# Kernel tuning notes

Hardware: AMD Instinct MI355X
Metric: run time of the kernel (lower is better)

Reference implementation:

```python
import jax, jax.numpy as jnp
import numpy as np

AUX_LOSS_WEIGHT = 0.01
TOP_K = 2


def setup_inputs() -> dict:
    key = jax.random.key(0)
    k0, k1, k2, k3, k4 = jax.random.split(key, 5)
    B, S, H, I, E = 4, 2048, 1024, 2816, 8
    scale = 0.02
    x = jax.random.normal(k0, (B, S, H), dtype=jnp.float32)
    Wr = jax.random.normal(k1, (H, E), dtype=jnp.float32) * scale   # router
    Wg = jax.random.normal(k2, (E, H, I), dtype=jnp.float32) * scale  # gate proj per expert
    Wu = jax.random.normal(k3, (E, H, I), dtype=jnp.float32) * scale  # up proj per expert
    Wd = jax.random.normal(k4, (E, I, H), dtype=jnp.float32) * scale  # down proj per expert
    return {"x": x, "Wr": Wr, "Wg": Wg, "Wu": Wu, "Wd": Wd}


def reference(x, Wr, Wg, Wu, Wd):
    B, S, H = x.shape
    E = Wr.shape[1]
    xf = x.reshape(-1, H)                      # [T, H]

    # Router: softmax -> top-k -> renormalize top-k weights
    logits = xf @ Wr                           # [T, E]
    probs = jax.nn.softmax(logits, axis=-1)
    vals, idx = jax.lax.top_k(probs, TOP_K)    # [T, K]
    vals = vals / (vals.sum(axis=-1, keepdims=True) + 1e-9)

    # Aux load-balancing loss (matches torch: mean prob * mean one-hot load)
    oh = jax.nn.one_hot(idx, E, dtype=xf.dtype)        # [T, K, E]
    expert_load = oh.sum(axis=1).mean(axis=0)          # [E]
    expert_prob = probs.mean(axis=0)                   # [E]
    router_loss = E * jnp.sum(expert_prob * expert_load) * AUX_LOSS_WEIGHT

    # Per-token combine weight for each expert: c[t,e] = sum_k vals[t,k] * (idx[t,k]==e)
    comb = jnp.einsum('tk,tke->te', vals, oh)          # [T, E]

    # Loop over the small fixed set of experts (dense SwiGLU, masked-weighted combine;
    # identical math to gather -> expert -> weighted index_add scatter)
    def expert_step(acc, ew):
        wg, wu, wd, ce = ew                            # [H,I], [H,I], [I,H], [T]
        h = jax.nn.silu(xf @ wg) * (xf @ wu)           # [T, I]
        return acc + (h @ wd) * ce[:, None], None

    out, _ = jax.lax.scan(expert_step, jnp.zeros_like(xf), (Wg, Wu, Wd, comb.T))
    return out.reshape(B, S, H), router_loss
```

## Files before the change

### kernel.cpp

```cpp
#include <hip/hip_runtime.h>
#include <stdint.h>

#define T_TOK 8192
#define HD    1024
#define ID    2816
#define NE    8
#define RCAP  17408

typedef __bf16 bf16x8 __attribute__((ext_vector_type(8)));
typedef float  f32x4  __attribute__((ext_vector_type(4)));

__device__ __forceinline__ unsigned short f2bf(float f) {
  union { float f; unsigned u; } v; v.f = f;
  unsigned r = v.u + 0x7FFFu + ((v.u >> 16) & 1u);
  return (unsigned short)(r >> 16);
}

__device__ __forceinline__ void gl16(const void* g, void* l) {
  __builtin_amdgcn_global_load_lds((__attribute__((address_space(1))) void*)g,
                                   (__attribute__((address_space(3))) void*)l,
                                   16, 0, 0);
}

__global__ void k_cvt_x(const float* __restrict__ x, unsigned short* __restrict__ xb) {
  const int i = blockIdx.x * blockDim.x + threadIdx.x;
  const float4 v = ((const float4*)x)[i];
  ushort4 o;
  o.x = f2bf(v.x); o.y = f2bf(v.y); o.z = f2bf(v.z); o.w = f2bf(v.w);
  ((ushort4*)xb)[i] = o;
}

__global__ void k_transpose(const float* __restrict__ Wg, const float* __restrict__ Wu,
                            const float* __restrict__ Wd,
                            unsigned short* __restrict__ Wgt, unsigned short* __restrict__ Wut,
                            unsigned short* __restrict__ Wdt) {
  const int m = blockIdx.y;
  const float* src; unsigned short* dst; int R, C;
  if (m < 8)       { src = Wg + (size_t)m * HD * ID;        dst = Wgt + (size_t)m * HD * ID;        R = HD; C = ID; }
  else if (m < 16) { src = Wu + (size_t)(m - 8) * HD * ID;  dst = Wut + (size_t)(m - 8) * HD * ID;  R = HD; C = ID; }
  else             { src = Wd + (size_t)(m - 16) * HD * ID; dst = Wdt + (size_t)(m - 16) * HD * ID; R = ID; C = HD; }
  const int tc = C / 64;
  const int tr = blockIdx.x / tc, tcc = blockIdx.x % tc;
  const int r0 = tr * 64, c0 = tcc * 64;
  __shared__ __align__(16) unsigned short tl[64 * 64];
  const int t = threadIdx.x;
  const int rb = t >> 4;
  const int c4 = t & 15;
  const float* sp = src + (size_t)(r0 + rb * 4) * C + c0 + c4 * 4;
  float4 v[4];
#pragma unroll
  for (int i = 0; i < 4; ++i) v[i] = *(const float4*)(sp + (size_t)i * C);
  const float* vf = (const float*)v;
#pragma unroll
  for (int q = 0; q < 4; ++q) {
    const int c = c4 * 4 + q;
    ushort4 o;
    o.x = f2bf(vf[0 * 4 + q]); o.y = f2bf(vf[1 * 4 + q]);
    o.z = f2bf(vf[2 * 4 + q]); o.w = f2bf(vf[3 * 4 + q]);
    *(ushort4*)&tl[c * 64 + ((rb ^ (c & 15)) * 4)] = o;
  }
  __syncthreads();
  const int orow = t >> 2, seg = t & 3;
  __align__(16) unsigned short tmp[16];
#pragma unroll
  for (int mI = 0; mI < 4; ++mI) {
    const int s = seg * 4 + mI;
    *(ushort4*)&tmp[mI * 4] = *(const ushort4*)&tl[orow * 64 + ((s ^ (orow & 15)) * 4)];
  }
  unsigned short* dp = dst + (size_t)(c0 + orow) * R + r0 + seg * 16;
  ((uint4*)dp)[0] = ((const uint4*)tmp)[0];
  ((uint4*)dp)[1] = ((const uint4*)tmp)[1];
}

__global__ void k_router(const float* __restrict__ x, const float* __restrict__ Wr,
                         int* __restrict__ cnt, float* __restrict__ psum,
                         int* __restrict__ tok_e, float* __restrict__ tok_w) {
  __shared__ float bp[NE];
  __shared__ int bc[NE];
  const int tid = threadIdx.x;
  if (tid < NE) { bp[tid] = 0.f; bc[tid] = 0; }
  __syncthreads();
  const int lane = tid & 63, w = tid >> 6;
  const int t = blockIdx.x * 4 + w;
  float acc[NE] = {0.f, 0.f, 0.f, 0.f, 0.f, 0.f, 0.f, 0.f};
  for (int h = lane; h < HD; h += 64) {
    const float xv = x[(size_t)t * HD + h];
    const float4 w0 = *(const float4*)(Wr + h * 8);
    const float4 w1 = *(const float4*)(Wr + h * 8 + 4);
    acc[0] += xv * w0.x; acc[1] += xv * w0.y; acc[2] += xv * w0.z; acc[3] += xv * w0.w;
    acc[4] += xv * w1.x; acc[5] += xv * w1.y; acc[6] += xv * w1.z; acc[7] += xv * w1.w;
  }
#pragma unroll
  for (int e = 0; e < NE; ++e)
    for (int off = 32; off > 0; off >>= 1)
      acc[e] += __shfl_xor(acc[e], off, 64);
  if (lane == 0) {
    float mx = acc[0];
    for (int e = 1; e < NE; ++e) mx = fmaxf(mx, acc[e]);
    float p[NE], s = 0.f;
    for (int e = 0; e < NE; ++e) { p[e] = __expf(acc[e] - mx); s += p[e]; }
    const float inv = 1.f / s;
    for (int e = 0; e < NE; ++e) p[e] *= inv;
    int e0 = 0;
    for (int e = 1; e < NE; ++e) if (p[e] > p[e0]) e0 = e;
    int e1 = (e0 == 0) ? 1 : 0;
    for (int e = 0; e < NE; ++e) if (e != e0 && p[e] > p[e1]) e1 = e;
    const float v0 = p[e0], v1 = p[e1];
    const float invs = 1.f / (v0 + v1 + 1e-9f);
    tok_e[2 * t] = e0;          tok_e[2 * t + 1] = e1;
    tok_w[2 * t] = v0 * invs;   tok_w[2 * t + 1] = v1 * invs;
    atomicAdd(&bc[e0], 1); atomicAdd(&bc[e1], 1);
    for (int e = 0; e < NE; ++e) atomicAdd(&bp[e], p[e]);
  }
  __syncthreads();
  if (tid < NE) { atomicAdd(&cnt[tid], bc[tid]); atomicAdd(&psum[tid], bp[tid]); }
}

__global__ void k_offsets(const int* __restrict__ cnt, const float* __restrict__ psum,
                          int* __restrict__ offp, int* __restrict__ pair_tok,
                          float* __restrict__ pair_w, float* __restrict__ loss_out) {
  __shared__ int soff[NE + 1], scnt[NE];
  if (threadIdx.x == 0) {
    int o = 0;
    for (int e = 0; e < NE; ++e) {
      soff[e] = o; scnt[e] = cnt[e];
      o += (scnt[e] + 127) & ~127;
    }
    soff[NE] = o;
    for (int e = 0; e <= NE; ++e) offp[e] = soff[e];
    float loss = 0.f;
    for (int e = 0; e < NE; ++e) loss += psum[e] * (float)scnt[e];
    loss *= (float)NE * 0.01f / ((float)T_TOK * (float)T_TOK);
    *loss_out = loss;
  }
  __syncthreads();
  for (int e = 0; e < NE; ++e) {
    const int base = soff[e] + scnt[e];
    const int n = soff[e + 1] - base;
    for (int j = threadIdx.x; j < n; j += blockDim.x) {
      pair_tok[base + j] = -1;
      pair_w[base + j] = 0.f;
    }
  }
}

__global__ void k_scatter(const int* __restrict__ tok_e, const float* __restrict__ tok_w,
                          const int* __restrict__ offp, int* __restrict__ cursor,
                          int* __restrict__ pair_tok, float* __restrict__ pair_w,
                          int* __restrict__ inv_p) {
  const int t = blockIdx.x * 256 + threadIdx.x;
#pragma unroll
  for (int k = 0; k < 2; ++k) {
    const int e = tok_e[2 * t + k];
    const int pos = atomicAdd(&cursor[e], 1);
    const int idx = offp[e] + pos;
    pair_tok[idx] = t;
    pair_w[idx] = tok_w[2 * t + k];
    inv_p[2 * t + k] = idx;
  }
}

__launch_bounds__(256, 2)
__global__ void k_stage1(const unsigned short* __restrict__ xb,
                         const unsigned short* __restrict__ Wgt,
                         const unsigned short* __restrict__ Wut,
                         const int* __restrict__ offp,
                         const int* __restrict__ pair_tok,
                         unsigned short* __restrict__ act) {
  __shared__ __align__(16) unsigned short lA[8192];
  __shared__ __align__(16) unsigned short lBg[8192];
  __shared__ __align__(16) unsigned short lBu[8192];
  __shared__ int toks[128];

  const int row0 = blockIdx.y * 128;
  if (row0 >= offp[8]) return;
  int e = 0;
  while (offp[e + 1] <= row0) ++e;
  const int i0 = blockIdx.x * 128;
  const int tid = threadIdx.x;
  if (tid < 128) {
    const int tk = pair_tok[row0 + tid];
    toks[tid] = tk < 0 ? 0 : tk;
  }
  __syncthreads();

  const int lane = tid & 63, w = tid >> 6;
  const unsigned short* gA[4];
  const unsigned short* gBg[4];
  const unsigned short* gBu[4];
  unsigned ldso[4];
  const unsigned short* wgtE = Wgt + (size_t)e * ID * HD;
  const unsigned short* wutE = Wut + (size_t)e * ID * HD;
#pragma unroll
  for (int j = 0; j < 4; ++j) {
    const int row = (w * 4 + j) * 8 + (lane >> 3);
    const int kb = (lane & 7) ^ (row & 7);
    gA[j]  = xb + (size_t)toks[row] * HD + kb * 8;
    gBg[j] = wgtE + (size_t)(i0 + row) * HD + kb * 8;
    gBu[j] = wutE + (size_t)(i0 + row) * HD + kb * 8;
    ldso[j] = (unsigned)(w * 4 + j) * 512u;
  }

  const f32x4 zero = {0.f, 0.f, 0.f, 0.f};
  f32x4 accg[4][4], accu[4][4];
#pragma unroll
  for (int a = 0; a < 4; ++a)
#pragma unroll
    for (int b = 0; b < 4; ++b) { accg[a][b] = zero; accu[a][b] = zero; }

  const int wm = (w & 1) * 64, wn = (w >> 1) * 64;
  const int colm = lane & 15, quad = lane >> 4;

  for (int kt = 0; kt < HD / 64; ++kt) {
    __syncthreads();
    const int ko = kt * 64;
#pragma unroll
    for (int j = 0; j < 4; ++j) {
      gl16(gA[j] + ko,  &lA[ldso[j]]);
      gl16(gBg[j] + ko, &lBg[ldso[j]]);
      gl16(gBu[j] + ko, &lBu[ldso[j]]);
    }
    __syncthreads();
#pragma unroll
    for (int kk = 0; kk < 2; ++kk) {
      const int kbl = kk * 4 + quad;
      bf16x8 af[4], bg[4], bu[4];
#pragma unroll
      for (int mf = 0; mf < 4; ++mf) {
        const int r = wm + mf * 16 + colm;
        af[mf] = *(const bf16x8*)&lA[r * 64 + ((kbl ^ (r & 7)) * 8)];
      }
#pragma unroll
      for (int nf = 0; nf < 4; ++nf) {
        const int r = wn + nf * 16 + colm;
        const int o = r * 64 + ((kbl ^ (r & 7)) * 8);
        bg[nf] = *(const bf16x8*)&lBg[o];
        bu[nf] = *(const bf16x8*)&lBu[o];
      }
#pragma unroll
      for (int mf = 0; mf < 4; ++mf)
#pragma unroll
        for (int nf = 0; nf < 4; ++nf) {
          accg[mf][nf] = __builtin_amdgcn_mfma_f32_16x16x32_bf16(af[mf], bg[nf], accg[mf][nf], 0, 0, 0);
          accu[mf][nf] = __builtin_amdgcn_mfma_f32_16x16x32_bf16(af[mf], bu[nf], accu[mf][nf], 0, 0, 0);
        }
    }
  }

#pragma unroll
  for (int mf = 0; mf < 4; ++mf) {
#pragma unroll
    for (int r = 0; r < 4; ++r) {
      const int orow = row0 + wm + mf * 16 + quad * 4 + r;
      unsigned short* arow = act + (size_t)orow * ID + i0 + wn + colm;
#pragma unroll
      for (int nf = 0; nf < 4; ++nf) {
        const float g = accg[mf][nf][r];
        const float u = accu[mf][nf][r];
        const float h = (g / (1.f + __expf(-g))) * u;
        arow[nf * 16] = f2bf(h);
      }
    }
  }
}

template <bool USE_CONTRIB>
__launch_bounds__(256, 2)
__global__ void k_stage2_t(const unsigned short* __restrict__ act,
                           const unsigned short* __restrict__ Wdt,
                           const int* __restrict__ offp,
                           const int* __restrict__ pair_tok,
                           const float* __restrict__ pair_w,
                           float* __restrict__ contrib,
                           float* __restrict__ out) {
  __shared__ __align__(16) unsigned short lA[8192];
  __shared__ __align__(16) unsigned short lB[8192];
  __shared__ int toks[128];
  __shared__ float wts[128];

  const int row0 = blockIdx.y * 128;
  if (row0 >= offp[8]) return;
  int e = 0;
  while (offp[e + 1] <= row0) ++e;
  const int h0 = blockIdx.x * 128;
  const int tid = threadIdx.x;
  if (!USE_CONTRIB && tid < 128) {
    toks[tid] = pair_tok[row0 + tid];
    wts[tid] = pair_w[row0 + tid];
  }
  const int lane = tid & 63, w = tid >> 6;
  const unsigned short* gA[4];
  const unsigned short* gB[4];
  unsigned ldso[4];
  const unsigned short* wdE = Wdt + (size_t)e * HD * ID;
#pragma unroll
  for (int j = 0; j < 4; ++j) {
    const int row = (w * 4 + j) * 8 + (lane >> 3);
    const int kb = (lane & 7) ^ (row & 7);
    gA[j] = act + (size_t)(row0 + row) * ID + kb * 8;
    gB[j] = wdE + (size_t)(h0 + row) * ID + kb * 8;
    ldso[j] = (unsigned)(w * 4 + j) * 512u;
  }

  const f32x4 zero = {0.f, 0.f, 0.f, 0.f};
  f32x4 acc[4][4];
#pragma unroll
  for (int a = 0; a < 4; ++a)
#pragma unroll
    for (int b = 0; b < 4; ++b) acc[a][b] = zero;

  const int wm = (w & 1) * 64, wn = (w >> 1) * 64;
  const int colm = lane & 15, quad = lane >> 4;

  for (int kt = 0; kt < ID / 64; ++kt) {
    __syncthreads();
    const int ko = kt * 64;
#pragma unroll
    for (int j = 0; j < 4; ++j) {
      gl16(gA[j] + ko, &lA[ldso[j]]);
      gl16(gB[j] + ko, &lB[ldso[j]]);
    }
    __syncthreads();
#pragma unroll
    for (int kk = 0; kk < 2; ++kk) {
      const int kbl = kk * 4 + quad;
      bf16x8 af[4], bf_[4];
#pragma unroll
      for (int mf = 0; mf < 4; ++mf) {
        const int r = wm + mf * 16 + colm;
        af[mf] = *(const bf16x8*)&lA[r * 64 + ((kbl ^ (r & 7)) * 8)];
      }
#pragma unroll
      for (int nf = 0; nf < 4; ++nf) {
        const int r = wn + nf * 16 + colm;
        bf_[nf] = *(const bf16x8*)&lB[r * 64 + ((kbl ^ (r & 7)) * 8)];
      }
#pragma unroll
      for (int mf = 0; mf < 4; ++mf)
#pragma unroll
        for (int nf = 0; nf < 4; ++nf)
          acc[mf][nf] = __builtin_amdgcn_mfma_f32_16x16x32_bf16(af[mf], bf_[nf], acc[mf][nf], 0, 0, 0);
    }
  }

#pragma unroll
  for (int mf = 0; mf < 4; ++mf) {
#pragma unroll
    for (int r = 0; r < 4; ++r) {
      const int lrow = wm + mf * 16 + quad * 4 + r;
      if (USE_CONTRIB) {
        float* crow = contrib + (size_t)(row0 + lrow) * HD + h0 + wn + colm;
#pragma unroll
        for (int nf = 0; nf < 4; ++nf)
          crow[nf * 16] = acc[mf][nf][r];
      } else {
        const int t = toks[lrow];
        if (t < 0) continue;
        const float wt = wts[lrow];
        float* orow = out + (size_t)t * HD + h0 + wn + colm;
#pragma unroll
        for (int nf = 0; nf < 4; ++nf)
          atomicAdd(&orow[nf * 16], wt * acc[mf][nf][r]);
      }
    }
  }
}

__global__ void k_combine(const float* __restrict__ contrib, const int* __restrict__ inv_p,
                          const float* __restrict__ tok_w, float* __restrict__ out) {
  const int t = blockIdx.x;
  const int h4 = threadIdx.x;
  const int p0 = inv_p[2 * t], p1 = inv_p[2 * t + 1];
  const float w0 = tok_w[2 * t], w1 = tok_w[2 * t + 1];
  const float4 a = ((const float4*)(contrib + (size_t)p0 * HD))[h4];
  const float4 b = ((const float4*)(contrib + (size_t)p1 * HD))[h4];
  float4 o;
  o.x = w0 * a.x + w1 * b.x;
  o.y = w0 * a.y + w1 * b.y;
  o.z = w0 * a.z + w1 * b.z;
  o.w = w0 * a.w + w1 * b.w;
  ((float4*)(out + (size_t)t * HD))[h4] = o;
}

extern "C" void kernel_launch(void* const* d_in, const int* in_sizes, int n_in,
                              void* d_out, int out_size, void* d_ws, size_t ws_size,
                              hipStream_t stream) {
  const float* x  = (const float*)d_in[0];
  const float* Wr = (const float*)d_in[1];
  const float* Wg = (const float*)d_in[2];
  const float* Wu = (const float*)d_in[3];
  const float* Wd = (const float*)d_in[4];
  float* out = (float*)d_out;

  char* ws = (char*)d_ws;
  const size_t off_xb  = 256;
  const size_t sz_xb   = (size_t)T_TOK * HD * 2;
  const size_t sz_w    = (size_t)NE * HD * ID * 2;
  const size_t off_wgt = off_xb + sz_xb;
  const size_t off_wut = off_wgt + sz_w;
  const size_t off_wdt = off_wut + sz_w;
  const size_t off_act = off_wdt + sz_w;
  const size_t sz_act  = (size_t)RCAP * ID * 2;
  const size_t off_ptk = off_act + sz_act;
  const size_t off_pw  = off_ptk + (size_t)RCAP * 4;
  const size_t off_te  = off_pw + (size_t)RCAP * 4;
  const size_t off_tw  = off_te + (size_t)T_TOK * 2 * 4;
  const size_t off_ip  = off_tw + (size_t)T_TOK * 2 * 4;
  const size_t off_ctb = off_ip + (size_t)T_TOK * 2 * 4;
  const size_t need_base = off_ctb;
  const size_t need_full = off_ctb + (size_t)RCAP * HD * 4;
  if (ws_size < need_base) return;
  const bool use_contrib = (ws_size >= need_full);

  int*   cnt    = (int*)(ws + 0);
  float* psum   = (float*)(ws + 32);
  int*   cursor = (int*)(ws + 64);
  int*   offp   = (int*)(ws + 96);
  unsigned short* xb  = (unsigned short*)(ws + off_xb);
  unsigned short* Wgt = (unsigned short*)(ws + off_wgt);
  unsigned short* Wut = (unsigned short*)(ws + off_wut);
  unsigned short* Wdt = (unsigned short*)(ws + off_wdt);
  unsigned short* act = (unsigned short*)(ws + off_act);
  int*   pair_tok = (int*)(ws + off_ptk);
  float* pair_w   = (float*)(ws + off_pw);
  int*   tok_e    = (int*)(ws + off_te);
  float* tok_w    = (float*)(ws + off_tw);
  int*   inv_p    = (int*)(ws + off_ip);
  float* contrib  = (float*)(ws + off_ctb);

  hipMemsetAsync(ws, 0, 256, stream);
  if (!use_contrib)
    hipMemsetAsync(out, 0, (size_t)T_TOK * HD * sizeof(float), stream);

  k_cvt_x<<<(T_TOK * HD / 4) / 256, 256, 0, stream>>>(x, xb);
  k_transpose<<<dim3(704, 24), 256, 0, stream>>>(Wg, Wu, Wd, Wgt, Wut, Wdt);
  k_router<<<T_TOK / 4, 256, 0, stream>>>(x, Wr, cnt, psum, tok_e, tok_w);
  k_offsets<<<1, 256, 0, stream>>>(cnt, psum, offp, pair_tok, pair_w, out + (size_t)T_TOK * HD);
  k_scatter<<<T_TOK / 256, 256, 0, stream>>>(tok_e, tok_w, offp, cursor, pair_tok, pair_w, inv_p);
  k_stage1<<<dim3(ID / 128, RCAP / 128), 256, 0, stream>>>(xb, Wgt, Wut, offp, pair_tok, act);
  if (use_contrib) {
    k_stage2_t<true><<<dim3(HD / 128, RCAP / 128), 256, 0, stream>>>(act, Wdt, offp, pair_tok, pair_w, contrib, out);
    k_combine<<<T_TOK, 256, 0, stream>>>(contrib, inv_p, tok_w, out);
  } else {
    k_stage2_t<false><<<dim3(HD / 128, RCAP / 128), 256, 0, stream>>>(act, Wdt, offp, pair_tok, pair_w, contrib, out);
  }
}
```

Baseline: 832.3 us.

## Pipeline grouped GEMMs with double-buffered LDS, 256-row tiles and XCD-aware block remap

Rewrites both expert GEMM kernels to use 512-thread blocks over 256x128 tiles. Each kernel has a double-buffered LDS ring with explicit vmcnt waits, raw s_barrier and setprio around MFMA bursts, so global-to-LDS loads overlap compute instead of sitting between two syncthreads. Expert segment padding rises to 256 rows (RCAP grows to match), and the grid is flattened with a swizzle that spreads consecutive blocks across XCDs. The extra padding adds some wasted rows, and the hand-counted waitcnt values are fragile if the load count per stage changes.

Result: slower. 1.100 ms (+32.1%).

```diff
diff --git a/kernel.cpp b/kernel.cpp
--- a/kernel.cpp
+++ b/kernel.cpp
@@ -5,7 +5,7 @@
 #define HD    1024
 #define ID    2816
 #define NE    8
-#define RCAP  17408
+#define RCAP  18432
 
 typedef __bf16 bf16x8 __attribute__((ext_vector_type(8)));
 typedef float  f32x4  __attribute__((ext_vector_type(4)));
@@ -21,6 +21,12 @@
                                    (__attribute__((address_space(3))) void*)l,
                                    16, 0, 0);
 }
+
+#define VMCNT(n) asm volatile("s_waitcnt vmcnt(" #n ")" ::: "memory")
+#define LGKM0    asm volatile("s_waitcnt lgkmcnt(0)" ::: "memory")
+#define BARRIER  do { __builtin_amdgcn_s_barrier(); asm volatile("" ::: "memory"); } while (0)
+#define PRIO1    __builtin_amdgcn_s_setprio(1)
+#define PRIO0    __builtin_amdgcn_s_setprio(0)
 
 __global__ void k_cvt_x(const float* __restrict__ x, unsigned short* __restrict__ xb) {
   const int i = blockIdx.x * blockDim.x + threadIdx.x;
@@ -124,7 +130,7 @@
     int o = 0;
     for (int e = 0; e < NE; ++e) {
       soff[e] = o; scnt[e] = cnt[e];
-      o += (scnt[e] + 127) & ~127;
+      o += (scnt[e] + 255) & ~255;
     }
     soff[NE] = o;
     for (int e = 0; e <= NE; ++e) offp[e] = soff[e];
@@ -160,45 +166,92 @@
   }
 }
 
-__launch_bounds__(256, 2)
+#define A_RG(b,h)  ((b) * 16384 + (h) * 8192)
+#define BG_RG(b,h) (32768 + (b) * 8192 + (h) * 4096)
+#define BU_RG(b,h) (49152 + (b) * 8192 + (h) * 4096)
+#define STG_A(b,h,t)  do { gl16(srcA0 + (t) * 64 + (h) * 32, &smem[A_RG(b,h) + wub]); \
+                           gl16(srcA1 + (t) * 64 + (h) * 32, &smem[A_RG(b,h) + 4096 + wub]); } while (0)
+#define STG_BG(b,h,t) gl16(srcBg + (t) * 64 + (h) * 32, &smem[BG_RG(b,h) + wub])
+#define STG_BU(b,h,t) gl16(srcBu + (t) * 64 + (h) * 32, &smem[BU_RG(b,h) + wub])
+
+#define S1_RD_AF(b,k) { _Pragma("unroll") for (int mf_ = 0; mf_ < 4; ++mf_) \
+                          af[mf_] = *(const bf16x8*)&smem[A_RG(b,k) + afoff[mf_]]; }
+#define S1_RD_BG(b,k) { _Pragma("unroll") for (int nf_ = 0; nf_ < 4; ++nf_) \
+                          bg[nf_] = *(const bf16x8*)&smem[BG_RG(b,k) + bnoff[nf_]]; }
+#define S1_RD_BU(b,k) { _Pragma("unroll") for (int nf_ = 0; nf_ < 4; ++nf_) \
+                          bu[nf_] = *(const bf16x8*)&smem[BU_RG(b,k) + bnoff[nf_]]; }
+#define S1_MM(ACC, BF) { _Pragma("unroll") for (int mf_ = 0; mf_ < 4; ++mf_) { \
+                           _Pragma("unroll") for (int nf_ = 0; nf_ < 4; ++nf_) \
+                             ACC[mf_][nf_] = __builtin_amdgcn_mfma_f32_16x16x32_bf16(af[mf_], BF[nf_], ACC[mf_][nf_], 0, 0, 0); } }
+
+#define S1_TILE(B, KT) do { \
+    bf16x8 af[4], bg[4], bu[4]; \
+     \
+    S1_RD_AF(B, 0); S1_RD_BG(B, 0); \
+    if ((KT) + 1 < 16) STG_BU((B) ^ 1, 1, (KT) + 1); \
+    BARRIER; LGKM0; PRIO1; S1_MM(accg, bg); PRIO0; BARRIER; \
+     \
+    S1_RD_BU(B, 0); \
+    if ((KT) + 2 < 16) { STG_A(B, 0, (KT) + 2); STG_BG(B, 0, (KT) + 2); } \
+    BARRIER; LGKM0; PRIO1; S1_MM(accu, bu); PRIO0; BARRIER; \
+     \
+    S1_RD_AF(B, 1); S1_RD_BG(B, 1); \
+    if ((KT) + 2 < 16) STG_BU(B, 0, (KT) + 2); \
+    BARRIER; LGKM0; PRIO1; S1_MM(accg, bg); PRIO0; BARRIER; \
+     \
+    S1_RD_BU(B, 1); \
+    if ((KT) + 2 < 16) { STG_A(B, 1, (KT) + 2); STG_BG(B, 1, (KT) + 2); } \
+    BARRIER; LGKM0; PRIO1; S1_MM(accu, bu); PRIO0; \
+    if ((KT) + 2 < 16) { VMCNT(7); } else { VMCNT(0); } \
+    BARRIER; \
+  } while (0)
+
+__launch_bounds__(512, 2)
 __global__ void k_stage1(const unsigned short* __restrict__ xb,
                          const unsigned short* __restrict__ Wgt,
                          const unsigned short* __restrict__ Wut,
                          const int* __restrict__ offp,
                          const int* __restrict__ pair_tok,
                          unsigned short* __restrict__ act) {
-  __shared__ __align__(16) unsigned short lA[8192];
-  __shared__ __align__(16) unsigned short lBg[8192];
-  __shared__ __align__(16) unsigned short lBu[8192];
-  __shared__ int toks[128];
-
-  const int row0 = blockIdx.y * 128;
+  __shared__ __align__(16) unsigned short smem[65536];
+  __shared__ int toks[256];
+
+  int wg = blockIdx.x;
+  wg = (wg & 7) * (1584 / 8) + (wg >> 3);
+  const int ytile = wg / 22, xtile = wg - ytile * 22;
+  const int row0 = ytile * 256;
   if (row0 >= offp[8]) return;
   int e = 0;
   while (offp[e + 1] <= row0) ++e;
-  const int i0 = blockIdx.x * 128;
+  const int i0 = xtile * 128;
+
   const int tid = threadIdx.x;
-  if (tid < 128) {
+  if (tid < 256) {
     const int tk = pair_tok[row0 + tid];
     toks[tid] = tk < 0 ? 0 : tk;
   }
   __syncthreads();
 
-  const int lane = tid & 63, w = tid >> 6;
-  const unsigned short* gA[4];
-  const unsigned short* gBg[4];
-  const unsigned short* gBu[4];
-  unsigned ldso[4];
+  const int l = tid & 63, w = tid >> 6;
+  const int colm = l & 15, quad = l >> 4;
+  const int wr = w >> 1, wc = w & 1;
+
+  const int rA0 = w * 16 + (l >> 2);
+  const int ks  = (l & 3) ^ ((l >> 2) & 3);
   const unsigned short* wgtE = Wgt + (size_t)e * ID * HD;
   const unsigned short* wutE = Wut + (size_t)e * ID * HD;
-#pragma unroll
-  for (int j = 0; j < 4; ++j) {
-    const int row = (w * 4 + j) * 8 + (lane >> 3);
-    const int kb = (lane & 7) ^ (row & 7);
-    gA[j]  = xb + (size_t)toks[row] * HD + kb * 8;
-    gBg[j] = wgtE + (size_t)(i0 + row) * HD + kb * 8;
-    gBu[j] = wutE + (size_t)(i0 + row) * HD + kb * 8;
-    ldso[j] = (unsigned)(w * 4 + j) * 512u;
+  const unsigned short* srcA0 = xb + (size_t)toks[rA0] * HD + ks * 8;
+  const unsigned short* srcA1 = xb + (size_t)toks[rA0 + 128] * HD + ks * 8;
+  const unsigned short* srcBg = wgtE + (size_t)(i0 + rA0) * HD + ks * 8;
+  const unsigned short* srcBu = wutE + (size_t)(i0 + rA0) * HD + ks * 8;
+  const int wub = w * 512;
+
+  const int sl = (quad ^ (colm & 3)) * 8;
+  int afoff[4], bnoff[4];
+#pragma unroll
+  for (int i = 0; i < 4; ++i) {
+    afoff[i] = (wr * 64 + i * 16 + colm) * 32 + sl;
+    bnoff[i] = (wc * 64 + i * 16 + colm) * 32 + sl;
   }
 
   const f32x4 zero = {0.f, 0.f, 0.f, 0.f};
@@ -208,51 +261,23 @@
 #pragma unroll
     for (int b = 0; b < 4; ++b) { accg[a][b] = zero; accu[a][b] = zero; }
 
-  const int wm = (w & 1) * 64, wn = (w >> 1) * 64;
-  const int colm = lane & 15, quad = lane >> 4;
-
-  for (int kt = 0; kt < HD / 64; ++kt) {
-    __syncthreads();
-    const int ko = kt * 64;
-#pragma unroll
-    for (int j = 0; j < 4; ++j) {
-      gl16(gA[j] + ko,  &lA[ldso[j]]);
-      gl16(gBg[j] + ko, &lBg[ldso[j]]);
-      gl16(gBu[j] + ko, &lBu[ldso[j]]);
-    }
-    __syncthreads();
-#pragma unroll
-    for (int kk = 0; kk < 2; ++kk) {
-      const int kbl = kk * 4 + quad;
-      bf16x8 af[4], bg[4], bu[4];
-#pragma unroll
-      for (int mf = 0; mf < 4; ++mf) {
-        const int r = wm + mf * 16 + colm;
-        af[mf] = *(const bf16x8*)&lA[r * 64 + ((kbl ^ (r & 7)) * 8)];
-      }
-#pragma unroll
-      for (int nf = 0; nf < 4; ++nf) {
-        const int r = wn + nf * 16 + colm;
-        const int o = r * 64 + ((kbl ^ (r & 7)) * 8);
-        bg[nf] = *(const bf16x8*)&lBg[o];
-        bu[nf] = *(const bf16x8*)&lBu[o];
-      }
-#pragma unroll
-      for (int mf = 0; mf < 4; ++mf)
-#pragma unroll
-        for (int nf = 0; nf < 4; ++nf) {
-          accg[mf][nf] = __builtin_amdgcn_mfma_f32_16x16x32_bf16(af[mf], bg[nf], accg[mf][nf], 0, 0, 0);
-          accu[mf][nf] = __builtin_amdgcn_mfma_f32_16x16x32_bf16(af[mf], bu[nf], accu[mf][nf], 0, 0, 0);
-        }
-    }
+  STG_A(0, 0, 0); STG_BG(0, 0, 0); STG_BU(0, 0, 0);
+  STG_A(0, 1, 0); STG_BG(0, 1, 0); STG_BU(0, 1, 0);
+  STG_A(1, 0, 1); STG_BG(1, 0, 1); STG_BU(1, 0, 1);
+  STG_A(1, 1, 1); STG_BG(1, 1, 1);
+  VMCNT(7); BARRIER;
+
+  for (int kt = 0; kt < 16; kt += 2) {
+    S1_TILE(0, kt);
+    S1_TILE(1, kt + 1);
   }
 
 #pragma unroll
   for (int mf = 0; mf < 4; ++mf) {
 #pragma unroll
     for (int r = 0; r < 4; ++r) {
-      const int orow = row0 + wm + mf * 16 + quad * 4 + r;
-      unsigned short* arow = act + (size_t)orow * ID + i0 + wn + colm;
+      const int orow = row0 + wr * 64 + mf * 16 + quad * 4 + r;
+      unsigned short* arow = act + (size_t)orow * ID + i0 + wc * 64 + colm;
 #pragma unroll
       for (int nf = 0; nf < 4; ++nf) {
         const float g = accg[mf][nf][r];
@@ -264,8 +289,38 @@
   }
 }
 
+#define A2_RG(b,h) ((b) * 16384 + (h) * 8192)
+#define B2_RG(b,h) (32768 + (b) * 8192 + (h) * 4096)
+#define STG2_A(b,h,t) do { gl16(srcA0 + (t) * 64 + (h) * 32, &smem[A2_RG(b,h) + wub]); \
+                           gl16(srcA1 + (t) * 64 + (h) * 32, &smem[A2_RG(b,h) + 4096 + wub]); } while (0)
+#define STG2_B(b,h,t) gl16(srcB + (t) * 64 + (h) * 32, &smem[B2_RG(b,h) + wub])
+
+#define S2_RD_AF(b,k) { _Pragma("unroll") for (int mf_ = 0; mf_ < 4; ++mf_) \
+                          af[mf_] = *(const bf16x8*)&smem[A2_RG(b,k) + afoff[mf_]]; }
+#define S2_RD_BF(b,k) { _Pragma("unroll") for (int nf_ = 0; nf_ < 4; ++nf_) \
+                          bf_[nf_] = *(const bf16x8*)&smem[B2_RG(b,k) + bnoff[nf_]]; }
+#define S2_MM { _Pragma("unroll") for (int mf_ = 0; mf_ < 4; ++mf_) { \
+                  _Pragma("unroll") for (int nf_ = 0; nf_ < 4; ++nf_) \
+                    acc[mf_][nf_] = __builtin_amdgcn_mfma_f32_16x16x32_bf16(af[mf_], bf_[nf_], acc[mf_][nf_], 0, 0, 0); } }
+
+#define S2_TILE(B, T) do { \
+    bf16x8 af[4], bf_[4]; \
+     \
+    S2_RD_AF(B, 0); S2_RD_BF(B, 0); \
+    if ((T) + 1 < 44) { STG2_A((B) ^ 1, 1, (T) + 1); STG2_B((B) ^ 1, 1, (T) + 1); } \
+    BARRIER; LGKM0; PRIO1; S2_MM; PRIO0; \
+    if ((T) + 1 < 44) { VMCNT(6); } else { VMCNT(0); } \
+    BARRIER; \
+     \
+    S2_RD_AF(B, 1); S2_RD_BF(B, 1); \
+    if ((T) + 2 < 44) { STG2_A(B, 0, (T) + 2); STG2_B(B, 0, (T) + 2); } \
+    BARRIER; LGKM0; PRIO1; S2_MM; PRIO0; \
+    if ((T) + 2 < 44) { VMCNT(6); } else if ((T) + 1 < 44) { VMCNT(3); } else { VMCNT(0); } \
+    BARRIER; \
+  } while (0)
+
 template <bool USE_CONTRIB>
-__launch_bounds__(256, 2)
+__launch_bounds__(512, 2)
 __global__ void k_stage2_t(const unsigned short* __restrict__ act,
                            const unsigned short* __restrict__ Wdt,
                            const int* __restrict__ offp,
@@ -273,33 +328,40 @@
                            const float* __restrict__ pair_w,
                            float* __restrict__ contrib,
                            float* __restrict__ out) {
-  __shared__ __align__(16) unsigned short lA[8192];
-  __shared__ __align__(16) unsigned short lB[8192];
-  __shared__ int toks[128];
-  __shared__ float wts[128];
-
-  const int row0 = blockIdx.y * 128;
+  __shared__ __align__(16) unsigned short smem[49152];
+  __shared__ int toks[256];
+  __shared__ float wts[256];
+
+  int wg = blockIdx.x;
+  wg = (wg & 7) * (576 / 8) + (wg >> 3);
+  const int ytile = wg >> 3, xtile = wg & 7;
+  const int row0 = ytile * 256;
   if (row0 >= offp[8]) return;
   int e = 0;
   while (offp[e + 1] <= row0) ++e;
-  const int h0 = blockIdx.x * 128;
+  const int h0 = xtile * 128;
   const int tid = threadIdx.x;
-  if (!USE_CONTRIB && tid < 128) {
+  if (!USE_CONTRIB && tid < 256) {
     toks[tid] = pair_tok[row0 + tid];
     wts[tid] = pair_w[row0 + tid];
   }
-  const int lane = tid & 63, w = tid >> 6;
-  const unsigned short* gA[4];
-  const unsigned short* gB[4];
-  unsigned ldso[4];
+
+  const int l = tid & 63, w = tid >> 6;
+  const int colm = l & 15, quad = l >> 4;
+  const int wr = w >> 1, wc = w & 1;
+  const int rA0 = w * 16 + (l >> 2);
+  const int ks = (l & 3) ^ ((l >> 2) & 3);
   const unsigned short* wdE = Wdt + (size_t)e * HD * ID;
-#pragma unroll
-  for (int j = 0; j < 4; ++j) {
-    const int row = (w * 4 + j) * 8 + (lane >> 3);
-    const int kb = (lane & 7) ^ (row & 7);
-    gA[j] = act + (size_t)(row0 + row) * ID + kb * 8;
-    gB[j] = wdE + (size_t)(h0 + row) * ID + kb * 8;
-    ldso[j] = (unsigned)(w * 4 + j) * 512u;
+  const unsigned short* srcA0 = act + (size_t)(row0 + rA0) * ID + ks * 8;
+  const unsigned short* srcA1 = act + (size_t)(row0 + rA0 + 128) * ID + ks * 8;
+  const unsigned short* srcB  = wdE + (size_t)(h0 + rA0) * ID + ks * 8;
+  const int wub = w * 512;
+  const int sl = (quad ^ (colm & 3)) * 8;
+  int afoff[4], bnoff[4];
+#pragma unroll
+  for (int i = 0; i < 4; ++i) {
+    afoff[i] = (wr * 64 + i * 16 + colm) * 32 + sl;
+    bnoff[i] = (wc * 64 + i * 16 + colm) * 32 + sl;
   }
 
   const f32x4 zero = {0.f, 0.f, 0.f, 0.f};
@@ -309,47 +371,23 @@
 #pragma unroll
     for (int b = 0; b < 4; ++b) acc[a][b] = zero;
 
-  const int wm = (w & 1) * 64, wn = (w >> 1) * 64;
-  const int colm = lane & 15, quad = lane >> 4;
-
-  for (int kt = 0; kt < ID / 64; ++kt) {
-    __syncthreads();
-    const int ko = kt * 64;
-#pragma unroll
-    for (int j = 0; j < 4; ++j) {
-      gl16(gA[j] + ko, &lA[ldso[j]]);
-      gl16(gB[j] + ko, &lB[ldso[j]]);
-    }
-    __syncthreads();
-#pragma unroll
-    for (int kk = 0; kk < 2; ++kk) {
-      const int kbl = kk * 4 + quad;
-      bf16x8 af[4], bf_[4];
-#pragma unroll
-      for (int mf = 0; mf < 4; ++mf) {
-        const int r = wm + mf * 16 + colm;
-        af[mf] = *(const bf16x8*)&lA[r * 64 + ((kbl ^ (r & 7)) * 8)];
-      }
-#pragma unroll
-      for (int nf = 0; nf < 4; ++nf) {
-        const int r = wn + nf * 16 + colm;
-        bf_[nf] = *(const bf16x8*)&lB[r * 64 + ((kbl ^ (r & 7)) * 8)];
-      }
-#pragma unroll
-      for (int mf = 0; mf < 4; ++mf)
-#pragma unroll
-        for (int nf = 0; nf < 4; ++nf)
-          acc[mf][nf] = __builtin_amdgcn_mfma_f32_16x16x32_bf16(af[mf], bf_[nf], acc[mf][nf], 0, 0, 0);
-    }
+  STG2_A(0, 0, 0); STG2_B(0, 0, 0);
+  STG2_A(0, 1, 0); STG2_B(0, 1, 0);
+  STG2_A(1, 0, 1); STG2_B(1, 0, 1);
+  VMCNT(3); BARRIER;
+
+  for (int T = 0; T < 44; T += 2) {
+    S2_TILE(0, T);
+    S2_TILE(1, T + 1);
   }
 
 #pragma unroll
   for (int mf = 0; mf < 4; ++mf) {
 #pragma unroll
     for (int r = 0; r < 4; ++r) {
-      const int lrow = wm + mf * 16 + quad * 4 + r;
+      const int lrow = wr * 64 + mf * 16 + quad * 4 + r;
       if (USE_CONTRIB) {
-        float* crow = contrib + (size_t)(row0 + lrow) * HD + h0 + wn + colm;
+        float* crow = contrib + (size_t)(row0 + lrow) * HD + h0 + wc * 64 + colm;
 #pragma unroll
         for (int nf = 0; nf < 4; ++nf)
           crow[nf * 16] = acc[mf][nf][r];
@@ -357,7 +395,7 @@
         const int t = toks[lrow];
         if (t < 0) continue;
         const float wt = wts[lrow];
-        float* orow = out + (size_t)t * HD + h0 + wn + colm;
+        float* orow = out + (size_t)t * HD + h0 + wc * 64 + colm;
 #pragma unroll
         for (int nf = 0; nf < 4; ++nf)
           atomicAdd(&orow[nf * 16], wt * acc[mf][nf][r]);
@@ -437,11 +475,11 @@
   k_router<<<T_TOK / 4, 256, 0, stream>>>(x, Wr, cnt, psum, tok_e, tok_w);
   k_offsets<<<1, 256, 0, stream>>>(cnt, psum, offp, pair_tok, pair_w, out + (size_t)T_TOK * HD);
   k_scatter<<<T_TOK / 256, 256, 0, stream>>>(tok_e, tok_w, offp, cursor, pair_tok, pair_w, inv_p);
-  k_stage1<<<dim3(ID / 128, RCAP / 128), 256, 0, stream>>>(xb, Wgt, Wut, offp, pair_tok, act);
+  k_stage1<<<(ID / 128) * (RCAP / 256), 512, 0, stream>>>(xb, Wgt, Wut, offp, pair_tok, act);
   if (use_contrib) {
-    k_stage2_t<true><<<dim3(HD / 128, RCAP / 128), 256, 0, stream>>>(act, Wdt, offp, pair_tok, pair_w, contrib, out);
+    k_stage2_t<true><<<(HD / 128) * (RCAP / 256), 512, 0, stream>>>(act, Wdt, offp, pair_tok, pair_w, contrib, out);
     k_combine<<<T_TOK, 256, 0, stream>>>(contrib, inv_p, tok_w, out);
   } else {
-    k_stage2_t<false><<<dim3(HD / 128, RCAP / 128), 256, 0, stream>>>(act, Wdt, offp, pair_tok, pair_w, contrib, out);
-  }
-}
+    k_stage2_t<false><<<(HD / 128) * (RCAP / 256), 512, 0, stream>>>(act, Wdt, offp, pair_tok, pair_w, contrib, out);
+  }
+}
```
